# Performance work log

Measured on AMD Instinct MI355X. Metric: run time of the kernel, lower is better.

Reference implementation:

```python
import jax, jax.numpy as jnp
import numpy as np

B, L1, L2 = 16, 32, 128
DEC = 512       # decoder_size
MEM = 512       # memory_bank_size
TOP = 50        # topic_num


def setup_inputs() -> dict:
    key = jax.random.key(0)
    ks = jax.random.split(key, 16)
    s = lambda fan_in: 1.0 / np.sqrt(fan_in)
    inp = {
        "decoder_state": jax.random.normal(ks[0], (B, DEC), jnp.float32),
        "doc_memory": jax.random.normal(ks[1], (B, L1, MEM), jnp.float32),
        "word_memory": jax.random.normal(ks[2], (B, L1, L2, MEM), jnp.float32),
        "topic_dist": jax.random.uniform(ks[3], (B, TOP), jnp.float32),
        "doc_mask": jnp.ones((B, L1), jnp.int32),
        "word_mask": jnp.ones((B, L1, L2), jnp.int32),
        # HierAttention params (PyTorch Linear weight layout: [out, in])
        "Wv": jax.random.uniform(ks[4], (1, DEC), jnp.float32, -s(DEC), s(DEC)),
        "Wd": jax.random.uniform(ks[5], (DEC, DEC), jnp.float32, -s(DEC), s(DEC)),
        "Wt": jax.random.uniform(ks[6], (DEC, TOP), jnp.float32, -s(TOP), s(TOP)),
        "Wm": jax.random.uniform(ks[7], (DEC, MEM), jnp.float32, -s(MEM), s(MEM)),
        # doc_attention (inner Attention) params
        "Wv2": jax.random.uniform(ks[8], (1, DEC), jnp.float32, -s(DEC), s(DEC)),
        "Wd2": jax.random.uniform(ks[9], (DEC, DEC), jnp.float32, -s(DEC), s(DEC)),
        "Wt2": jax.random.uniform(ks[10], (DEC, TOP), jnp.float32, -s(TOP), s(TOP)),
        "Wm2": jax.random.uniform(ks[11], (DEC, MEM), jnp.float32, -s(MEM), s(MEM)),
    }
    return inp


def reference(decoder_state, doc_memory, word_memory, topic_dist,
              doc_mask, word_mask,
              Wv, Wd, Wt, Wm, Wv2, Wd2, Wt2, Wm2):
    neg_inf = jnp.float32(-jnp.inf)

    # ---- word-level (HierAttention.score) ----
    enc_feat = jnp.einsum('bqwm,dm->bqwd', word_memory, Wm)      # [B,L1,L2,DEC]
    dec_feat = decoder_state @ Wd.T                              # [B,DEC]
    top_feat = topic_dist @ Wt.T                                 # [B,DEC]
    e = jnp.tanh(enc_feat + (dec_feat + top_feat)[:, None, None, :])
    word_scores = jnp.einsum('bqwd,od->bqw', e, Wv)[..., 0] if Wv.shape[0] != 1 else jnp.einsum('bqwd,d->bqw', e, Wv[0])
    word_scores = jnp.where(word_mask == 0, neg_inf, word_scores)
    word_attn = jax.nn.softmax(word_scores, axis=-1)             # [B,L1,L2]

    # ---- doc-level (Attention.score) ----
    enc_feat_d = jnp.einsum('bqm,dm->bqd', doc_memory, Wm2)      # [B,L1,DEC]
    dec_feat_d = decoder_state @ Wd2.T                           # [B,DEC]
    top_feat_d = topic_dist @ Wt2.T                              # [B,DEC]
    e_d = jnp.tanh(enc_feat_d + (dec_feat_d + top_feat_d)[:, None, :])
    doc_scores = jnp.einsum('bqd,d->bq', e_d, Wv2[0])            # [B,L1]
    doc_scores = jnp.where(doc_mask == 0, neg_inf, doc_scores)
    doc_attn = jax.nn.softmax(doc_scores, axis=-1)               # [B,L1]

    # ---- combine ----
    rescaled = doc_attn[..., None] * word_attn                   # [B,L1,L2]
    context = jnp.einsum('bqw,bqwm->bm', rescaled, word_memory)  # [B,MEM]
    return context, rescaled
```

## Files before the change

kernel.cpp:

```cpp
#include <hip/hip_runtime.h>
#include <hip/hip_bf16.h>
#include <math.h>

#define BATCH 16
#define L1 32
#define L2 128
#define DEC 512
#define MEM 512
#define TOPN 50
#define NROWS (BATCH * L1 * L2)
#define NBQ (BATCH * L1)

typedef short short8 __attribute__((ext_vector_type(8)));
typedef float f32x16 __attribute__((ext_vector_type(16)));

#define WS_WP     0
#define WS_WP2    131072
#define WS_BIAS1  262144
#define WS_BIAS2  270336
#define WS_DOCSC  278528

__device__ __forceinline__ unsigned int pkbf(float a, float b) {
    __hip_bfloat162 h = __float22bfloat162_rn(float2{a, b});
    union { __hip_bfloat162 h; unsigned int u; } c{h};
    return c.u;
}

__device__ __forceinline__ float fast_tanh(float x) {
    return 1.f - 2.f / (__expf(2.f * x) + 1.f);
}

__global__ __launch_bounds__(256) void setup_kernel(
    const float* __restrict__ Wm, const float* __restrict__ Wm2,
    unsigned short* __restrict__ Wp, unsigned short* __restrict__ Wp2,
    const float* __restrict__ dec, const float* __restrict__ topic,
    const float* __restrict__ Wd, const float* __restrict__ Wt,
    const float* __restrict__ Wd2, const float* __restrict__ Wt2,
    float* __restrict__ bias1, float* __restrict__ bias2,
    float* __restrict__ ctx_out)
{
    if (blockIdx.x < 128) {
        int s = blockIdx.x * 256 + threadIdx.x;
        int C = s >> 10;
        int u = s & 1023;
        int nt = u >> 6, k8 = (u >> 5) & 1, n_in = u & 31;
        int d = nt * 32 + n_in;
        int k = C * 16 + k8 * 8;

        const float* src = Wm + (size_t)d * DEC + k;
        uint4 v;
        v.x = pkbf(src[0], src[1]); v.y = pkbf(src[2], src[3]);
        v.z = pkbf(src[4], src[5]); v.w = pkbf(src[6], src[7]);
        ((uint4*)Wp)[s] = v;

        const float* src2 = Wm2 + (size_t)d * DEC + k;
        uint4 w;
        w.x = pkbf(src2[0], src2[1]); w.y = pkbf(src2[2], src2[3]);
        w.z = pkbf(src2[4], src2[5]); w.w = pkbf(src2[6], src2[7]);
        ((uint4*)Wp2)[s] = w;
    } else if (blockIdx.x < 160) {
        int idx = (blockIdx.x - 128) * 256 + threadIdx.x;
        int b = idx >> 9, d = idx & 511;
        float a1 = 0.f, a2 = 0.f;
        const float* db = dec + b * DEC;
        const float* w1 = Wd + (size_t)d * DEC;
        const float* w2 = Wd2 + (size_t)d * DEC;
#pragma unroll 4
        for (int k = 0; k < DEC; ++k) {
            float x = db[k];
            a1 = fmaf(x, w1[k], a1);
            a2 = fmaf(x, w2[k], a2);
        }
        const float* tb = topic + b * TOPN;
        const float* t1 = Wt + (size_t)d * TOPN;
        const float* t2 = Wt2 + (size_t)d * TOPN;
#pragma unroll 2
        for (int t = 0; t < TOPN; ++t) {
            float x = tb[t];
            a1 = fmaf(x, t1[t], a1);
            a2 = fmaf(x, t2[t], a2);
        }
        bias1[idx] = a1;
        bias2[idx] = a2;
    } else {
        int i = (blockIdx.x - 160) * 256 + threadIdx.x;
        float4 z = {0.f, 0.f, 0.f, 0.f};
        ((float4*)ctx_out)[i * 2] = z;
        ((float4*)ctx_out)[i * 2 + 1] = z;
    }
}

__global__ __launch_bounds__(256) void score_mfma_kernel(
    const float* __restrict__ X,
    const unsigned short* __restrict__ Wp,
    const float* __restrict__ Wv,
    const float* __restrict__ bias,
    float* __restrict__ scores,
    int bshift)
{
    __shared__ __align__(16) short lsA[256 * 8];
    __shared__ __align__(16) short lsB[2048 * 8];
    __shared__ float red[4][64];

    const int tid = threadIdx.x;
    const int lane = tid & 63;
    const int wid = tid >> 6;
    const int row0 = blockIdx.x * 64;

    const int srow = tid >> 2;
    const int kslot = tid & 3;
    const int sA = ((kslot >> 1) * 2 + (srow >> 5)) * 64 + (kslot & 1) * 32 + (srow & 31);
    const float4* xs4 = (const float4*)(X + (size_t)(row0 + srow) * DEC) + kslot * 2;

    const uint4* bsrc = (const uint4*)Wp + (size_t)wid * 512 + lane;

    f32x16 acc[8];
#pragma unroll
    for (int t = 0; t < 8; ++t)
        acc[t] = (f32x16){0.f,0.f,0.f,0.f, 0.f,0.f,0.f,0.f, 0.f,0.f,0.f,0.f, 0.f,0.f,0.f,0.f};

    const short8* lA = (const short8*)lsA;
    const short8* lB = (const short8*)lsB;

    for (int it = 0; it < 16; ++it) {
        uint4 bv[8];
#pragma unroll
        for (int i = 0; i < 8; ++i) bv[i] = bsrc[i * 64];
        bsrc += 2048;
#pragma unroll
        for (int i = 0; i < 8; ++i)
            *((uint4*)&lsB[((size_t)wid * 512 + i * 64 + lane) * 8]) = bv[i];

        float4 xv0 = xs4[0];
        float4 xv1 = xs4[1];
        xs4 += 8;
        union { unsigned int u[4]; short8 s; } xb;
        xb.u[0] = pkbf(xv0.x, xv0.y); xb.u[1] = pkbf(xv0.z, xv0.w);
        xb.u[2] = pkbf(xv1.x, xv1.y); xb.u[3] = pkbf(xv1.z, xv1.w);
        *((short8*)&lsA[sA * 8]) = xb.s;

        __syncthreads();

#pragma unroll
        for (int c = 0; c < 2; ++c) {
            short8 a0 = lA[(c * 2 + 0) * 64 + lane];
            short8 a1 = lA[(c * 2 + 1) * 64 + lane];
            short8 b0 = lB[c * 1024 + (wid * 4 + 0) * 64 + lane];
            short8 b1 = lB[c * 1024 + (wid * 4 + 1) * 64 + lane];
            short8 b2 = lB[c * 1024 + (wid * 4 + 2) * 64 + lane];
            short8 b3 = lB[c * 1024 + (wid * 4 + 3) * 64 + lane];
            acc[0] = __builtin_amdgcn_mfma_f32_32x32x16_bf16(a0, b0, acc[0], 0, 0, 0);
            acc[1] = __builtin_amdgcn_mfma_f32_32x32x16_bf16(a0, b1, acc[1], 0, 0, 0);
            acc[2] = __builtin_amdgcn_mfma_f32_32x32x16_bf16(a0, b2, acc[2], 0, 0, 0);
            acc[3] = __builtin_amdgcn_mfma_f32_32x32x16_bf16(a0, b3, acc[3], 0, 0, 0);
            acc[4] = __builtin_amdgcn_mfma_f32_32x32x16_bf16(a1, b0, acc[4], 0, 0, 0);
            acc[5] = __builtin_amdgcn_mfma_f32_32x32x16_bf16(a1, b1, acc[5], 0, 0, 0);
            acc[6] = __builtin_amdgcn_mfma_f32_32x32x16_bf16(a1, b2, acc[6], 0, 0, 0);
            acc[7] = __builtin_amdgcn_mfma_f32_32x32x16_bf16(a1, b3, acc[7], 0, 0, 0);
        }
        __syncthreads();
    }

    const int col = lane & 31;
    const int h = lane >> 5;
    float wv[4], bs[2][4];
    const int b0i = (row0) >> bshift;
    const int b1i = (row0 + 32) >> bshift;
#pragma unroll
    for (int nt = 0; nt < 4; ++nt) {
        int d = wid * 128 + nt * 32 + col;
        wv[nt] = Wv[d];
        bs[0][nt] = bias[b0i * DEC + d];
        bs[1][nt] = bias[b1i * DEC + d];
    }

#pragma unroll
    for (int mt = 0; mt < 2; ++mt) {
#pragma unroll
        for (int r = 0; r < 16; ++r) {
            float p = 0.f;
#pragma unroll
            for (int nt = 0; nt < 4; ++nt) {
                float x = acc[mt * 4 + nt][r] + bs[mt][nt];
                p = fmaf(wv[nt], fast_tanh(x), p);
            }
            p += __shfl_xor(p, 16);
            p += __shfl_xor(p, 8);
            p += __shfl_xor(p, 4);
            p += __shfl_xor(p, 2);
            p += __shfl_xor(p, 1);
            if (col == mt * 16 + r) {
                int row_in = (r & 3) + 8 * (r >> 2) + 4 * h;
                red[wid][mt * 32 + row_in] = p;
            }
        }
    }
    __syncthreads();
    if (tid < 64)
        scores[row0 + tid] = red[0][tid] + red[1][tid] + red[2][tid] + red[3][tid];
}

__global__ __launch_bounds__(512) void fused_word_kernel(
    const float* __restrict__ X,
    const unsigned short* __restrict__ Wp,
    const float* __restrict__ Wv,
    const float* __restrict__ bias1,
    const float* __restrict__ doc_scores,
    const int* __restrict__ doc_mask,
    const int* __restrict__ word_mask,
    float* __restrict__ rescaled_out,
    float* __restrict__ ctx_out)
{
    __shared__ __align__(16) short lsA[2 * 2048];
    __shared__ float red[8][128];
    __shared__ float sS[128];
    __shared__ float rmax2[2], rsum2[2];
    __shared__ float s_dattn;
    __shared__ __align__(16) float4 part[3 * 128];

    const int tid = threadIdx.x;
    const int lane = tid & 63;
    const int wid = tid >> 6;
    const int bq = blockIdx.x;
    const int r0 = bq * L2;
    const int b = bq >> 5;
    const int q = bq & 31;

    if (tid < 32) {
        int di = b * 32 + tid;
        float dsv = doc_scores[di];
        if (doc_mask[di] == 0) dsv = -INFINITY;
        float mx = dsv;
#pragma unroll
        for (int o = 1; o <= 16; o <<= 1) mx = fmaxf(mx, __shfl_xor(mx, o));
        float e = __expf(dsv - mx);
        float sum = e;
#pragma unroll
        for (int o = 1; o <= 16; o <<= 1) sum += __shfl_xor(sum, o);
        if (tid == q) s_dattn = e / sum;
    }

    const int row = tid >> 2;
    const int kq = tid & 3;
    const int mt_s = row >> 5;
    const int rl_s = row & 31;
    const int k8_s = kq >> 1;
    const int q4 = (kq & 1) * 4;
    const int slot_s = mt_s * 64 + k8_s * 32 + rl_s;
    const float4* xs = (const float4*)(X + (size_t)(r0 + row) * DEC) + kq;

    const uint4* Bp = (const uint4*)Wp;
    const int boff = wid * 128 + lane;

    f32x16 acc[8];
#pragma unroll
    for (int t = 0; t < 8; ++t)
        acc[t] = (f32x16){0.f,0.f,0.f,0.f, 0.f,0.f,0.f,0.f, 0.f,0.f,0.f,0.f, 0.f,0.f,0.f,0.f};

    const short8* lA = (const short8*)lsA;

    float4 va[4];
#pragma unroll
    for (int i = 0; i < 4; ++i) va[i] = xs[i * 4];
    uint4 ub0[2], ub1[2];
#pragma unroll
    for (int i = 0; i < 2; ++i) {
        ub0[i] = Bp[i * 1024 + boff];
        ub1[i] = Bp[i * 1024 + boff + 64];
    }

#pragma unroll
    for (int c = 0; c < 32; ++c) {
        const int p = c & 1;
        const int ia = c & 3;
        uint2 w2;
        w2.x = pkbf(va[ia].x, va[ia].y);
        w2.y = pkbf(va[ia].z, va[ia].w);
        *(uint2*)&lsA[(p * 256 + slot_s) * 8 + q4] = w2;
        __syncthreads();

        va[ia] = xs[((c + 4) & 31) * 4];
        uint4 nb0 = Bp[((c + 2) & 31) * 1024 + boff];
        uint4 nb1 = Bp[((c + 2) & 31) * 1024 + boff + 64];

        short8 a0 = lA[p * 256 + 0 * 64 + lane];
        short8 a1 = lA[p * 256 + 1 * 64 + lane];
        short8 a2 = lA[p * 256 + 2 * 64 + lane];
        short8 a3 = lA[p * 256 + 3 * 64 + lane];
        union { uint4 u; short8 s; } cb0{ub0[p]}, cb1{ub1[p]};
        acc[0] = __builtin_amdgcn_mfma_f32_32x32x16_bf16(a0, cb0.s, acc[0], 0, 0, 0);
        acc[1] = __builtin_amdgcn_mfma_f32_32x32x16_bf16(a0, cb1.s, acc[1], 0, 0, 0);
        acc[2] = __builtin_amdgcn_mfma_f32_32x32x16_bf16(a1, cb0.s, acc[2], 0, 0, 0);
        acc[3] = __builtin_amdgcn_mfma_f32_32x32x16_bf16(a1, cb1.s, acc[3], 0, 0, 0);
        acc[4] = __builtin_amdgcn_mfma_f32_32x32x16_bf16(a2, cb0.s, acc[4], 0, 0, 0);
        acc[5] = __builtin_amdgcn_mfma_f32_32x32x16_bf16(a2, cb1.s, acc[5], 0, 0, 0);
        acc[6] = __builtin_amdgcn_mfma_f32_32x32x16_bf16(a3, cb0.s, acc[6], 0, 0, 0);
        acc[7] = __builtin_amdgcn_mfma_f32_32x32x16_bf16(a3, cb1.s, acc[7], 0, 0, 0);

        ub0[p] = nb0; ub1[p] = nb1;
    }

    const int col = lane & 31;
    const int h = lane >> 5;
    float wv0, wv1, bs0, bs1;
    {
        int d0 = wid * 64 + col;
        int d1 = wid * 64 + 32 + col;
        wv0 = Wv[d0]; wv1 = Wv[d1];
        bs0 = bias1[b * DEC + d0]; bs1 = bias1[b * DEC + d1];
    }
#pragma unroll
    for (int mt = 0; mt < 4; ++mt) {
#pragma unroll
        for (int r = 0; r < 16; ++r) {
            float p = fmaf(wv0, fast_tanh(acc[mt * 2 + 0][r] + bs0),
                           wv1 * fast_tanh(acc[mt * 2 + 1][r] + bs1));
            p += __shfl_xor(p, 16);
            p += __shfl_xor(p, 8);
            p += __shfl_xor(p, 4);
            p += __shfl_xor(p, 2);
            p += __shfl_xor(p, 1);
            if (col == r) {
                int row_in = (r & 3) + 8 * (r >> 2) + 4 * h;
                red[wid][mt * 32 + row_in] = p;
            }
        }
    }
    __syncthreads();

    float e = 0.f, sv = 0.f;
    if (tid < 128) {
        sv = red[0][tid] + red[1][tid] + red[2][tid] + red[3][tid]
           + red[4][tid] + red[5][tid] + red[6][tid] + red[7][tid];
        if (word_mask[r0 + tid] == 0) sv = -INFINITY;
        float mx = sv;
#pragma unroll
        for (int o = 1; o <= 32; o <<= 1) mx = fmaxf(mx, __shfl_xor(mx, o));
        if (lane == 0) rmax2[wid] = mx;
    }
    __syncthreads();
    if (tid < 128) {
        float mx = fmaxf(rmax2[0], rmax2[1]);
        e = __expf(sv - mx);
        float sum = e;
#pragma unroll
        for (int o = 1; o <= 32; o <<= 1) sum += __shfl_xor(sum, o);
        if (lane == 0) rsum2[wid] = sum;
    }
    __syncthreads();
    if (tid < 128) {
        float sum = rsum2[0] + rsum2[1];
        float resc = s_dattn * (e / sum);
        sS[tid] = resc;
        rescaled_out[r0 + tid] = resc;
    }
    __syncthreads();

    const int hh = tid >> 7;
    const int m4 = tid & 127;
    const float4* Xr = (const float4*)X + (size_t)r0 * 128 + (size_t)hh * 32 * 128 + m4;
    float4 a = {0.f, 0.f, 0.f, 0.f};
#pragma unroll 8
    for (int i = 0; i < 32; ++i) {
        float rr = sS[hh * 32 + i];
        float4 v = Xr[(size_t)i * 128];
        a.x = fmaf(rr, v.x, a.x);
        a.y = fmaf(rr, v.y, a.y);
        a.z = fmaf(rr, v.z, a.z);
        a.w = fmaf(rr, v.w, a.w);
    }
    if (hh) part[(hh - 1) * 128 + m4] = a;
    __syncthreads();
    if (hh == 0) {
        float4 p0 = part[m4], p1 = part[128 + m4], p2 = part[256 + m4];
        a.x += p0.x + p1.x + p2.x;
        a.y += p0.y + p1.y + p2.y;
        a.z += p0.z + p1.z + p2.z;
        a.w += p0.w + p1.w + p2.w;
        float* dst = ctx_out + (size_t)b * MEM + m4 * 4;
        atomicAdd(dst + 0, a.x);
        atomicAdd(dst + 1, a.y);
        atomicAdd(dst + 2, a.z);
        atomicAdd(dst + 3, a.w);
    }
}

extern "C" void kernel_launch(void* const* d_in, const int* in_sizes, int n_in,
                              void* d_out, int out_size, void* d_ws, size_t ws_size,
                              hipStream_t stream) {
    const float* decoder_state = (const float*)d_in[0];
    const float* doc_memory    = (const float*)d_in[1];
    const float* word_memory   = (const float*)d_in[2];
    const float* topic_dist    = (const float*)d_in[3];
    const int*   doc_mask      = (const int*)d_in[4];
    const int*   word_mask     = (const int*)d_in[5];
    const float* Wv  = (const float*)d_in[6];
    const float* Wd  = (const float*)d_in[7];
    const float* Wt  = (const float*)d_in[8];
    const float* Wm  = (const float*)d_in[9];
    const float* Wv2 = (const float*)d_in[10];
    const float* Wd2 = (const float*)d_in[11];
    const float* Wt2 = (const float*)d_in[12];
    const float* Wm2 = (const float*)d_in[13];

    float* ws = (float*)d_ws;
    unsigned short* Wp  = (unsigned short*)(ws + WS_WP);
    unsigned short* Wp2 = (unsigned short*)(ws + WS_WP2);
    float* bias1       = ws + WS_BIAS1;
    float* bias2       = ws + WS_BIAS2;
    float* doc_scores  = ws + WS_DOCSC;

    float* ctx_out      = (float*)d_out;
    float* rescaled_out = (float*)d_out + BATCH * MEM;

    setup_kernel<<<164, 256, 0, stream>>>(Wm, Wm2, Wp, Wp2,
                                          decoder_state, topic_dist,
                                          Wd, Wt, Wd2, Wt2, bias1, bias2, ctx_out);
    score_mfma_kernel<<<NBQ / 64, 256, 0, stream>>>(doc_memory, Wp2, Wv2, bias2, doc_scores, 5);
    fused_word_kernel<<<NBQ, 512, 0, stream>>>(word_memory, Wp, Wv, bias1,
                                               doc_scores, doc_mask, word_mask,
                                               rescaled_out, ctx_out);
}
```

Measured before the change: 351.7 us.

## Stage whole bf16 word tile in LDS and reuse it for context sum

The word kernel now converts the block's full 128x512 word-memory tile to bf16 and stores it in LDS (128 KB) in two halves, replacing the per-chunk double-buffered streaming. The context reduction then reads the bf16 tile from LDS instead of re-reading fp32 X from global memory, removing a second pass over the largest input. This costs occupancy (one block per CU given LDS size) and fewer overlap opportunities between loads and MFMA, and the context now uses bf16-rounded memory values, which reduces accuracy.

```diff
diff --git a/kernel.cpp b/kernel.cpp
--- a/kernel.cpp
+++ b/kernel.cpp
@@ -211,12 +211,11 @@
     float* __restrict__ rescaled_out,
     float* __restrict__ ctx_out)
 {
-    __shared__ __align__(16) short lsA[2 * 2048];
+    __shared__ __align__(16) short lsA[2][32768];
     __shared__ float red[8][128];
     __shared__ float sS[128];
     __shared__ float rmax2[2], rsum2[2];
     __shared__ float s_dattn;
-    __shared__ __align__(16) float4 part[3 * 128];
 
     const int tid = threadIdx.x;
     const int lane = tid & 63;
@@ -240,14 +239,13 @@
         if (tid == q) s_dattn = e / sum;
     }
 
-    const int row = tid >> 2;
+    const int r = tid >> 2;
     const int kq = tid & 3;
-    const int mt_s = row >> 5;
-    const int rl_s = row & 31;
-    const int k8_s = kq >> 1;
-    const int q4 = (kq & 1) * 4;
-    const int slot_s = mt_s * 64 + k8_s * 32 + rl_s;
-    const float4* xs = (const float4*)(X + (size_t)(r0 + row) * DEC) + kq;
+    const int mt_s = r >> 5;
+    const int rl_s = r & 31;
+    const int lpart = (kq >> 1) * 32 + rl_s;
+    const int j0 = (kq & 1) * 4;
+    const float4* xrow = (const float4*)(X + (size_t)(r0 + r) * DEC);
 
     const uint4* Bp = (const uint4*)Wp;
     const int boff = wid * 128 + lane;
@@ -257,11 +255,6 @@
     for (int t = 0; t < 8; ++t)
         acc[t] = (f32x16){0.f,0.f,0.f,0.f, 0.f,0.f,0.f,0.f, 0.f,0.f,0.f,0.f, 0.f,0.f,0.f,0.f};
 
-    const short8* lA = (const short8*)lsA;
-
-    float4 va[4];
-#pragma unroll
-    for (int i = 0; i < 4; ++i) va[i] = xs[i * 4];
     uint4 ub0[2], ub1[2];
 #pragma unroll
     for (int i = 0; i < 2; ++i) {
@@ -270,34 +263,46 @@
     }
 
 #pragma unroll
-    for (int c = 0; c < 32; ++c) {
-        const int p = c & 1;
-        const int ia = c & 3;
-        uint2 w2;
-        w2.x = pkbf(va[ia].x, va[ia].y);
-        w2.y = pkbf(va[ia].z, va[ia].w);
-        *(uint2*)&lsA[(p * 256 + slot_s) * 8 + q4] = w2;
+    for (int kc = 0; kc < 2; ++kc) {
+#pragma unroll
+        for (int hf = 0; hf < 2; ++hf) {
+            float4 va[8];
+#pragma unroll
+            for (int i = 0; i < 8; ++i)
+                va[i] = xrow[kc * 64 + hf * 32 + i * 4 + kq];
+#pragma unroll
+            for (int i = 0; i < 8; ++i) {
+                int c = hf * 8 + i;
+                uint2 w2;
+                w2.x = pkbf(va[i].x, va[i].y);
+                w2.y = pkbf(va[i].z, va[i].w);
+                *(uint2*)&lsA[kc][((c * 4 + mt_s) * 64 + lpart) * 8 + j0] = w2;
+            }
+        }
         __syncthreads();
 
-        va[ia] = xs[((c + 4) & 31) * 4];
-        uint4 nb0 = Bp[((c + 2) & 31) * 1024 + boff];
-        uint4 nb1 = Bp[((c + 2) & 31) * 1024 + boff + 64];
-
-        short8 a0 = lA[p * 256 + 0 * 64 + lane];
-        short8 a1 = lA[p * 256 + 1 * 64 + lane];
-        short8 a2 = lA[p * 256 + 2 * 64 + lane];
-        short8 a3 = lA[p * 256 + 3 * 64 + lane];
-        union { uint4 u; short8 s; } cb0{ub0[p]}, cb1{ub1[p]};
-        acc[0] = __builtin_amdgcn_mfma_f32_32x32x16_bf16(a0, cb0.s, acc[0], 0, 0, 0);
-        acc[1] = __builtin_amdgcn_mfma_f32_32x32x16_bf16(a0, cb1.s, acc[1], 0, 0, 0);
-        acc[2] = __builtin_amdgcn_mfma_f32_32x32x16_bf16(a1, cb0.s, acc[2], 0, 0, 0);
-        acc[3] = __builtin_amdgcn_mfma_f32_32x32x16_bf16(a1, cb1.s, acc[3], 0, 0, 0);
-        acc[4] = __builtin_amdgcn_mfma_f32_32x32x16_bf16(a2, cb0.s, acc[4], 0, 0, 0);
-        acc[5] = __builtin_amdgcn_mfma_f32_32x32x16_bf16(a2, cb1.s, acc[5], 0, 0, 0);
-        acc[6] = __builtin_amdgcn_mfma_f32_32x32x16_bf16(a3, cb0.s, acc[6], 0, 0, 0);
-        acc[7] = __builtin_amdgcn_mfma_f32_32x32x16_bf16(a3, cb1.s, acc[7], 0, 0, 0);
-
-        ub0[p] = nb0; ub1[p] = nb1;
+        const short8* lAp = (const short8*)lsA[kc];
+#pragma unroll
+        for (int c = 0; c < 16; ++c) {
+            const int p = c & 1;
+            short8 a0 = lAp[(c * 4 + 0) * 64 + lane];
+            short8 a1 = lAp[(c * 4 + 1) * 64 + lane];
+            short8 a2 = lAp[(c * 4 + 2) * 64 + lane];
+            short8 a3 = lAp[(c * 4 + 3) * 64 + lane];
+            union { uint4 u; short8 s; } cb0{ub0[p]}, cb1{ub1[p]};
+            const int C2 = (kc * 16 + c + 2) & 31;
+            uint4 nb0 = Bp[C2 * 1024 + boff];
+            uint4 nb1 = Bp[C2 * 1024 + boff + 64];
+            acc[0] = __builtin_amdgcn_mfma_f32_32x32x16_bf16(a0, cb0.s, acc[0], 0, 0, 0);
+            acc[1] = __builtin_amdgcn_mfma_f32_32x32x16_bf16(a0, cb1.s, acc[1], 0, 0, 0);
+            acc[2] = __builtin_amdgcn_mfma_f32_32x32x16_bf16(a1, cb0.s, acc[2], 0, 0, 0);
+            acc[3] = __builtin_amdgcn_mfma_f32_32x32x16_bf16(a1, cb1.s, acc[3], 0, 0, 0);
+            acc[4] = __builtin_amdgcn_mfma_f32_32x32x16_bf16(a2, cb0.s, acc[4], 0, 0, 0);
+            acc[5] = __builtin_amdgcn_mfma_f32_32x32x16_bf16(a2, cb1.s, acc[5], 0, 0, 0);
+            acc[6] = __builtin_amdgcn_mfma_f32_32x32x16_bf16(a3, cb0.s, acc[6], 0, 0, 0);
+            acc[7] = __builtin_amdgcn_mfma_f32_32x32x16_bf16(a3, cb1.s, acc[7], 0, 0, 0);
+            ub0[p] = nb0; ub1[p] = nb1;
+        }
     }
 
     const int col = lane & 31;
@@ -312,16 +317,16 @@
 #pragma unroll
     for (int mt = 0; mt < 4; ++mt) {
 #pragma unroll
-        for (int r = 0; r < 16; ++r) {
-            float p = fmaf(wv0, fast_tanh(acc[mt * 2 + 0][r] + bs0),
-                           wv1 * fast_tanh(acc[mt * 2 + 1][r] + bs1));
+        for (int rr = 0; rr < 16; ++rr) {
+            float p = fmaf(wv0, fast_tanh(acc[mt * 2 + 0][rr] + bs0),
+                           wv1 * fast_tanh(acc[mt * 2 + 1][rr] + bs1));
             p += __shfl_xor(p, 16);
             p += __shfl_xor(p, 8);
             p += __shfl_xor(p, 4);
             p += __shfl_xor(p, 2);
             p += __shfl_xor(p, 1);
-            if (col == r) {
-                int row_in = (r & 3) + 8 * (r >> 2) + 4 * h;
+            if (col == rr) {
+                int row_in = (rr & 3) + 8 * (rr >> 2) + 4 * h;
                 red[wid][mt * 32 + row_in] = p;
             }
         }
@@ -356,32 +361,23 @@
     }
     __syncthreads();
 
-    const int hh = tid >> 7;
-    const int m4 = tid & 127;
-    const float4* Xr = (const float4*)X + (size_t)r0 * 128 + (size_t)hh * 32 * 128 + m4;
-    float4 a = {0.f, 0.f, 0.f, 0.f};
-#pragma unroll 8
-    for (int i = 0; i < 32; ++i) {
-        float rr = sS[hh * 32 + i];
-        float4 v = Xr[(size_t)i * 128];
-        a.x = fmaf(rr, v.x, a.x);
-        a.y = fmaf(rr, v.y, a.y);
-        a.z = fmaf(rr, v.z, a.z);
-        a.w = fmaf(rr, v.w, a.w);
-    }
-    if (hh) part[(hh - 1) * 128 + m4] = a;
-    __syncthreads();
-    if (hh == 0) {
-        float4 p0 = part[m4], p1 = part[128 + m4], p2 = part[256 + m4];
-        a.x += p0.x + p1.x + p2.x;
-        a.y += p0.y + p1.y + p2.y;
-        a.z += p0.z + p1.z + p2.z;
-        a.w += p0.w + p1.w + p2.w;
-        float* dst = ctx_out + (size_t)b * MEM + m4 * 4;
-        atomicAdd(dst + 0, a.x);
-        atomicAdd(dst + 1, a.y);
-        atomicAdd(dst + 2, a.z);
-        atomicAdd(dst + 3, a.w);
+    {
+        const int m = tid;
+        const int kc = m >> 8;
+        const int mm = m & 255;
+        const int c = mm >> 4;
+        const int k8 = (mm >> 3) & 1;
+        const int j = mm & 7;
+        const unsigned short* Lp = (const unsigned short*)lsA[kc];
+        const int base = (c * 4) * 64 * 8 + (k8 * 32) * 8 + j;
+        float s = 0.f;
+#pragma unroll 4
+        for (int w = 0; w < 128; ++w) {
+            unsigned short u = Lp[base + ((w >> 5) * 64 + (w & 31)) * 8];
+            union { unsigned int ui; float f; } cv{(unsigned int)u << 16};
+            s = fmaf(sS[w], cv.f, s);
+        }
+        atomicAdd(ctx_out + (size_t)b * MEM + m, s);
     }
 }
 
```

Measured after the change: 359.3 us. 1.02x slower.
